# Optimization experiments

Measured on AMD Instinct MI355X. Metric: run time of the kernel, lower is better.

## Reference

```python
import jax, jax.numpy as jnp
import numpy as np

N_HEAD = 16

def setup_inputs() -> dict:
    key = jax.random.key(0)
    ks = jax.random.split(key, 9)
    C = 1024
    s = 1.0 / np.sqrt(C)
    x = jax.random.normal(ks[0], (2, 2048, C), dtype=jnp.float32)
    Wq = jax.random.normal(ks[1], (C, C), dtype=jnp.float32) * s
    Wk = jax.random.normal(ks[2], (C, C), dtype=jnp.float32) * s
    Wv = jax.random.normal(ks[3], (C, C), dtype=jnp.float32) * s
    Wp = jax.random.normal(ks[4], (C, C), dtype=jnp.float32) * s
    z = jnp.zeros((C,), dtype=jnp.float32)
    return {"x": x, "Wq": Wq, "bq": z, "Wk": Wk, "bk": z, "Wv": Wv, "bv": z, "Wp": Wp, "bp": z}

def reference(x, Wq, bq, Wk, bk, Wv, bv, Wp, bp):
    B, T, C = x.shape
    H = N_HEAD
    D = C // H
    # QKV projections (Linear: x @ W.T + b), split heads -> [B, H, T, D]
    q = (x @ Wq.T + bq).reshape(B, T, H, D).transpose(0, 2, 1, 3)
    k = (x @ Wk.T + bk).reshape(B, T, H, D).transpose(0, 2, 1, 3)
    v = (x @ Wv.T + bv).reshape(B, T, H, D).transpose(0, 2, 1, 3)
    scale = 1.0 / jnp.sqrt(jnp.asarray(D, dtype=x.dtype))  # scaled_attn=True
    att = jnp.einsum('bhtd,bhsd->bhts', q, k) * scale      # [B,H,T,T]
    att = jax.nn.softmax(att, axis=-1)
    y = jnp.einsum('bhts,bhsd->bhtd', att, v)              # [B,H,T,D]
    y = y.transpose(0, 2, 1, 3).reshape(B, T, C)
    return y @ Wp.T + bp
```

## Files before the change

kernel.cpp:

```cpp
#include <hip/hip_runtime.h>
#include <stdint.h>

typedef unsigned short u16;
typedef __attribute__((ext_vector_type(8))) short short8;
typedef __attribute__((ext_vector_type(4))) float float4v;
typedef __attribute__((ext_vector_type(4))) u16 ushort4v;
typedef __attribute__((ext_vector_type(2))) unsigned int uint2v;

#define MFMA_BF16(a, b, c) __builtin_amdgcn_mfma_f32_16x16x32_bf16((a), (b), (c), 0, 0, 0)

__device__ __forceinline__ u16 f2bf(float f) {
    uint32_t u = __builtin_bit_cast(uint32_t, f);
    u += 0x7FFFu + ((u >> 16) & 1u);
    return (u16)(u >> 16);
}
__device__ __forceinline__ void g2l16(const void* g, void* l) {
    __builtin_amdgcn_global_load_lds(
        (const __attribute__((address_space(1))) void*)g,
        (__attribute__((address_space(3))) void*)l, 16, 0, 0);
}

__global__ void cast_all(const float* __restrict__ x, const float* __restrict__ wq,
                         const float* __restrict__ wk, const float* __restrict__ wv,
                         const float* __restrict__ wp,
                         u16* __restrict__ xb, u16* __restrict__ wqkvb, u16* __restrict__ wpb) {
    int bx = blockIdx.x;
    const float* src; u16* dst; int base;
    if (bx < 4096)      { src = x;  dst = xb;              base = bx; }
    else if (bx < 5120) { src = wq; dst = wqkvb;           base = bx - 4096; }
    else if (bx < 6144) { src = wk; dst = wqkvb + 1048576; base = bx - 5120; }
    else if (bx < 7168) { src = wv; dst = wqkvb + 2097152; base = bx - 6144; }
    else                { src = wp; dst = wpb;             base = bx - 7168; }
    int i = base * 1024 + threadIdx.x * 4;
    float4v v = *(const float4v*)(src + i);
    ushort4v o;
    #pragma unroll
    for (int r = 0; r < 4; ++r) o[r] = f2bf(v[r]);
    *(ushort4v*)(dst + i) = o;
}

__device__ __forceinline__ void gemm_core_128(const u16* __restrict__ A, const u16* __restrict__ B,
                                              int K, int m0, int n0, float4v acc[4][4]) {
    __shared__ u16 lA[128 * 64];
    __shared__ u16 lB[128 * 64];
    const int tid = threadIdx.x, lane = tid & 63;
    const int wave = tid >> 6, wm = wave >> 1, wn = wave & 1;
    const int l15 = lane & 15, quad = lane >> 4;

    for (int kt = 0; kt < K; kt += 64) {
        __syncthreads();
        #pragma unroll
        for (int i = 0; i < 4; ++i) {
            int f = i * 256 + tid;
            int row = f >> 3, kc = f & 7;
            g2l16(A + (size_t)(m0 + row) * K + kt + kc * 8, &lA[f * 8]);
            g2l16(B + (size_t)(n0 + row) * K + kt + kc * 8, &lB[f * 8]);
        }
        __syncthreads();
        #pragma unroll
        for (int ks = 0; ks < 2; ++ks) {
            short8 af[4], bf[4];
            #pragma unroll
            for (int t = 0; t < 4; ++t) {
                af[t] = *(const short8*)&lA[(wm * 64 + t * 16 + l15) * 64 + ks * 32 + quad * 8];
                bf[t] = *(const short8*)&lB[(wn * 64 + t * 16 + l15) * 64 + ks * 32 + quad * 8];
            }
            #pragma unroll
            for (int tm = 0; tm < 4; ++tm)
                #pragma unroll
                for (int tn = 0; tn < 4; ++tn)
                    acc[tm][tn] = MFMA_BF16(af[tm], bf[tn], acc[tm][tn]);
        }
    }
}

__global__ __launch_bounds__(256, 2) void gemm_qkv(
    const u16* __restrict__ xb, const u16* __restrict__ wqkv,
    const float* __restrict__ bq, const float* __restrict__ bk, const float* __restrict__ bv,
    u16* __restrict__ qo, u16* __restrict__ ko, u16* __restrict__ vto) {
    const int bx = blockIdx.x, by = blockIdx.y;
    const int tid = threadIdx.x, lane = tid & 63;
    const int wave = tid >> 6, wm = wave >> 1, wn = wave & 1;
    const int l15 = lane & 15, quad = lane >> 4;
    const float QSC = 0.125f * 1.44269504088896340736f;

    if (bx < 16) {
        float4v acc[4][4] = {};
        gemm_core_128(wqkv, xb, 1024, bx * 128, by * 128, acc);
        const bool isq = bx < 8;
        const float* bvec = isq ? bq : bk;
        u16* dst = isq ? qo : ko;
        #pragma unroll
        for (int tm = 0; tm < 4; ++tm) {
            int nloc = (bx & 7) * 128 + wm * 64 + tm * 16 + quad * 4;
            int h = nloc >> 6, d0 = nloc & 63;
            float4v bias = *(const float4v*)(bvec + nloc);
            #pragma unroll
            for (int tn = 0; tn < 4; ++tn) {
                int t = by * 128 + wn * 64 + tn * 16 + l15;
                int b = t >> 11, tt = t & 2047;
                ushort4v pk;
                #pragma unroll
                for (int r = 0; r < 4; ++r) {
                    float v = acc[tm][tn][r] + bias[r];
                    pk[r] = f2bf(isq ? v * QSC : v);
                }
                *(ushort4v*)&dst[(((size_t)(b * 16 + h)) * 2048 + tt) * 64 + d0] = pk;
            }
        }
    } else {
        float4v acc[4][4] = {};
        gemm_core_128(xb, wqkv, 1024, by * 128, bx * 128, acc);
        #pragma unroll
        for (int tn = 0; tn < 4; ++tn) {
            int n = bx * 128 + wn * 64 + tn * 16 + l15;
            int cb = n & 1023, h = cb >> 6, d = cb & 63;
            float bias = bv[cb];
            #pragma unroll
            for (int tm = 0; tm < 4; ++tm) {
                int mb = by * 128 + wm * 64 + tm * 16 + quad * 4;
                int b = mb >> 11, t0 = mb & 2047;
                ushort4v pk;
                #pragma unroll
                for (int r = 0; r < 4; ++r) pk[r] = f2bf(acc[tm][tn][r] + bias);
                *(ushort4v*)&vto[(((size_t)(b * 16 + h)) * 64 + d) * 2048 + t0] = pk;
            }
        }
    }
}

__global__ __launch_bounds__(256, 2) void gemm_out(
    const u16* __restrict__ yb, const u16* __restrict__ wpb,
    const float* __restrict__ bp, float* __restrict__ out) {
    float4v acc[4][4] = {};
    gemm_core_128(wpb, yb, 1024, blockIdx.x * 128, blockIdx.y * 128, acc);
    const int tid = threadIdx.x, lane = tid & 63;
    const int wave = tid >> 6, wm = wave >> 1, wn = wave & 1;
    const int l15 = lane & 15, quad = lane >> 4;
    #pragma unroll
    for (int tm = 0; tm < 4; ++tm) {
        int n = blockIdx.x * 128 + wm * 64 + tm * 16 + quad * 4;
        float4v bias = *(const float4v*)(bp + n);
        #pragma unroll
        for (int tn = 0; tn < 4; ++tn) {
            int t = blockIdx.y * 128 + wn * 64 + tn * 16 + l15;
            float4v o;
            #pragma unroll
            for (int r = 0; r < 4; ++r) o[r] = acc[tm][tn][r] + bias[r];
            *(float4v*)&out[(size_t)t * 1024 + n] = o;
        }
    }
}

__global__ __launch_bounds__(256, 2) void attn(
    const u16* __restrict__ qg, const u16* __restrict__ kg,
    const u16* __restrict__ vtg, u16* __restrict__ yb) {
    __shared__ u16 kbuf[128 * 64];
    __shared__ u16 pbuf[128 * 136];
    __shared__ float lsum[2][128];

    const int tid = threadIdx.x, lane = tid & 63;
    const int wave = tid >> 6;
    const int sm = wave >> 1, sn = wave & 1;
    const int mh = wave & 1, nh = wave >> 1;
    const int l15 = lane & 15, quad = lane >> 4;
    const int bh = blockIdx.y, qt0 = blockIdx.x * 128;

    const u16* qbase = qg + (size_t)bh * 2048 * 64;
    const u16* kbase = kg + (size_t)bh * 2048 * 64;
    const u16* vtbase = vtg + (size_t)bh * 64 * 2048;

    short8 qf[4][2];
    #pragma unroll
    for (int tn = 0; tn < 4; ++tn)
        #pragma unroll
        for (int ks = 0; ks < 2; ++ks)
            qf[tn][ks] = *(const short8*)(qbase + (size_t)(qt0 + sn * 64 + tn * 16 + l15) * 64 + ks * 32 + quad * 8);

    float4v oacc[2][4] = {};
    float rs[4] = {};

    for (int it = 0; it < 16; ++it) {
        const int kv0 = it * 128;
        __syncthreads();
        #pragma unroll
        for (int i = 0; i < 4; ++i) {
            int f = i * 256 + tid, row = f >> 3, kc = f & 7;
            g2l16(kbase + (size_t)(kv0 + row) * 64 + kc * 8, &kbuf[f * 8]);
        }
        short8 vf[4][2];
        #pragma unroll
        for (int kst = 0; kst < 4; ++kst)
            #pragma unroll
            for (int tmm = 0; tmm < 2; ++tmm)
                vf[kst][tmm] = *(const short8*)(vtbase + (size_t)(mh * 32 + tmm * 16 + l15) * 2048 + kv0 + kst * 32 + quad * 8);
        __syncthreads();
        float4v sacc[4][4] = {};
        #pragma unroll
        for (int ks = 0; ks < 2; ++ks) {
            short8 kf[4];
            #pragma unroll
            for (int tm = 0; tm < 4; ++tm)
                kf[tm] = *(const short8*)&kbuf[(sm * 64 + tm * 16 + l15) * 64 + ks * 32 + quad * 8];
            #pragma unroll
            for (int tm = 0; tm < 4; ++tm)
                #pragma unroll
                for (int tn = 0; tn < 4; ++tn)
                    sacc[tm][tn] = MFMA_BF16(kf[tm], qf[tn][ks], sacc[tm][tn]);
        }
        #pragma unroll
        for (int tm = 0; tm < 4; ++tm)
            #pragma unroll
            for (int tn = 0; tn < 4; ++tn) {
                uint32_t u[4];
                #pragma unroll
                for (int r = 0; r < 4; ++r) {
                    float p = __builtin_amdgcn_exp2f(sacc[tm][tn][r]);
                    u[r] = __builtin_bit_cast(uint32_t, p);
                    rs[tn] += __builtin_bit_cast(float, u[r] & 0xFFFF0000u);
                }
                uint2v pk;
                pk.x = __builtin_amdgcn_perm(u[1], u[0], 0x07060302u);
                pk.y = __builtin_amdgcn_perm(u[3], u[2], 0x07060302u);
                *(uint2v*)&pbuf[(sn * 64 + tn * 16 + l15) * 136 + sm * 64 + tm * 16 + quad * 4] = pk;
            }
        __syncthreads();
        #pragma unroll
        for (int kst = 0; kst < 4; ++kst) {
            short8 bfn[4];
            #pragma unroll
            for (int tnn = 0; tnn < 4; ++tnn)
                bfn[tnn] = *(const short8*)&pbuf[(nh * 64 + tnn * 16 + l15) * 136 + kst * 32 + quad * 8];
            #pragma unroll
            for (int tmm = 0; tmm < 2; ++tmm)
                #pragma unroll
                for (int tnn = 0; tnn < 4; ++tnn)
                    oacc[tmm][tnn] = MFMA_BF16(vf[kst][tmm], bfn[tnn], oacc[tmm][tnn]);
        }
    }
    #pragma unroll
    for (int tn = 0; tn < 4; ++tn) {
        float v = rs[tn];
        v += __shfl_xor(v, 16);
        v += __shfl_xor(v, 32);
        rs[tn] = v;
    }
    if (lane < 16)
        #pragma unroll
        for (int tn = 0; tn < 4; ++tn)
            lsum[sm][sn * 64 + tn * 16 + l15] = rs[tn];
    __syncthreads();
    const int b = bh >> 4, h = bh & 15;
    #pragma unroll
    for (int tnn = 0; tnn < 4; ++tnn) {
        int qrow = nh * 64 + tnn * 16 + l15;
        float inv = 1.0f / (lsum[0][qrow] + lsum[1][qrow]);
        #pragma unroll
        for (int tmm = 0; tmm < 2; ++tmm) {
            int d0 = mh * 32 + tmm * 16 + quad * 4;
            ushort4v pk;
            #pragma unroll
            for (int r = 0; r < 4; ++r) pk[r] = f2bf(oacc[tmm][tnn][r] * inv);
            *(ushort4v*)&yb[((size_t)(b * 2048 + qt0 + qrow)) * 1024 + h * 64 + d0] = pk;
        }
    }
}

extern "C" void kernel_launch(void* const* d_in, const int* in_sizes, int n_in,
                              void* d_out, int out_size, void* d_ws, size_t ws_size,
                              hipStream_t stream) {
    const float* x  = (const float*)d_in[0];
    const float* Wq = (const float*)d_in[1];
    const float* bq = (const float*)d_in[2];
    const float* Wk = (const float*)d_in[3];
    const float* bk = (const float*)d_in[4];
    const float* Wv = (const float*)d_in[5];
    const float* bv = (const float*)d_in[6];
    const float* Wp = (const float*)d_in[7];
    const float* bp = (const float*)d_in[8];
    float* out = (float*)d_out;
    uint8_t* ws = (uint8_t*)d_ws;

    u16* xb   = (u16*)(ws);
    u16* wqkv = (u16*)(ws + (8u << 20));
    u16* wpb  = (u16*)(ws + (14u << 20));
    u16* qb   = (u16*)(ws + (16u << 20));
    u16* kb   = (u16*)(ws + (24u << 20));
    u16* vtb  = (u16*)(ws + (32u << 20));
    u16* yb   = (u16*)(ws + (40u << 20));

    cast_all<<<8192, 256, 0, stream>>>(x, Wq, Wk, Wv, Wp, xb, wqkv, wpb);
    gemm_qkv<<<dim3(24, 32), 256, 0, stream>>>(xb, wqkv, bq, bk, bv, qb, kb, vtb);
    attn<<<dim3(16, 32), 256, 0, stream>>>(qb, kb, vtb, yb);
    gemm_out<<<dim3(8, 32), 256, 0, stream>>>(yb, wpb, bp, out);
}
```

Baseline: 209.6 us.

## Swizzle LDS tiles and restructure attention into split-KV waves with double buffering

The GEMM core and attention K tile now use an XOR swizzle on the LDS column index to avoid bank conflicts on MFMA fragment reads. The attention kernel shrinks the query tile to 64 rows and doubles the grid. Each wave takes a 32-key slice of every 128-key block, keeps its own P buffer (removing one block barrier per iteration), and double-buffers K loads. Partial outputs are reduced across the four waves through LDS at the end, which adds a final reduction step and more K/V reloads per query.

```diff
diff --git a/kernel.cpp b/kernel.cpp
--- a/kernel.cpp
+++ b/kernel.cpp
@@ -46,6 +46,7 @@
     const int tid = threadIdx.x, lane = tid & 63;
     const int wave = tid >> 6, wm = wave >> 1, wn = wave & 1;
     const int l15 = lane & 15, quad = lane >> 4;
+    const int sw7 = l15 & 7;
 
     for (int kt = 0; kt < K; kt += 64) {
         __syncthreads();
@@ -53,8 +54,9 @@
         for (int i = 0; i < 4; ++i) {
             int f = i * 256 + tid;
             int row = f >> 3, kc = f & 7;
-            g2l16(A + (size_t)(m0 + row) * K + kt + kc * 8, &lA[f * 8]);
-            g2l16(B + (size_t)(n0 + row) * K + kt + kc * 8, &lB[f * 8]);
+            int gcol = (kc ^ (row & 7)) * 8;
+            g2l16(A + (size_t)(m0 + row) * K + kt + gcol, &lA[f * 8]);
+            g2l16(B + (size_t)(n0 + row) * K + kt + gcol, &lB[f * 8]);
         }
         __syncthreads();
         #pragma unroll
@@ -62,8 +64,9 @@
             short8 af[4], bf[4];
             #pragma unroll
             for (int t = 0; t < 4; ++t) {
-                af[t] = *(const short8*)&lA[(wm * 64 + t * 16 + l15) * 64 + ks * 32 + quad * 8];
-                bf[t] = *(const short8*)&lB[(wn * 64 + t * 16 + l15) * 64 + ks * 32 + quad * 8];
+                int pc = ((ks * 4 + quad) ^ sw7) * 8;
+                af[t] = *(const short8*)&lA[(wm * 64 + t * 16 + l15) * 64 + pc];
+                bf[t] = *(const short8*)&lB[(wn * 64 + t * 16 + l15) * 64 + pc];
             }
             #pragma unroll
             for (int tm = 0; tm < 4; ++tm)
@@ -155,61 +158,67 @@
 __global__ __launch_bounds__(256, 2) void attn(
     const u16* __restrict__ qg, const u16* __restrict__ kg,
     const u16* __restrict__ vtg, u16* __restrict__ yb) {
-    __shared__ u16 kbuf[128 * 64];
-    __shared__ u16 pbuf[128 * 136];
-    __shared__ float lsum[2][128];
+    __shared__ __attribute__((aligned(16))) char smem[54272];
+    u16* kb0 = (u16*)smem;
+    u16* pb  = (u16*)(smem + 32768);
+    float* lsum = (float*)(smem + 53248);
+    float* red  = (float*)smem;
 
     const int tid = threadIdx.x, lane = tid & 63;
-    const int wave = tid >> 6;
-    const int sm = wave >> 1, sn = wave & 1;
-    const int mh = wave & 1, nh = wave >> 1;
-    const int l15 = lane & 15, quad = lane >> 4;
-    const int bh = blockIdx.y, qt0 = blockIdx.x * 128;
+    const int w = tid >> 6;
+    const int l15 = lane & 15, quad = lane >> 4, sw7 = l15 & 7;
+    const int bh = blockIdx.y, qt0 = blockIdx.x * 64;
 
     const u16* qbase = qg + (size_t)bh * 2048 * 64;
     const u16* kbase = kg + (size_t)bh * 2048 * 64;
     const u16* vtbase = vtg + (size_t)bh * 64 * 2048;
+    u16* pw = pb + w * 2560;
 
     short8 qf[4][2];
     #pragma unroll
     for (int tn = 0; tn < 4; ++tn)
         #pragma unroll
         for (int ks = 0; ks < 2; ++ks)
-            qf[tn][ks] = *(const short8*)(qbase + (size_t)(qt0 + sn * 64 + tn * 16 + l15) * 64 + ks * 32 + quad * 8);
-
-    float4v oacc[2][4] = {};
+            qf[tn][ks] = *(const short8*)(qbase + (size_t)(qt0 + tn * 16 + l15) * 64 + ks * 32 + quad * 8);
+
+    float4v oacc[4][4] = {};
     float rs[4] = {};
 
-    for (int it = 0; it < 16; ++it) {
-        const int kv0 = it * 128;
-        __syncthreads();
+    {
         #pragma unroll
         for (int i = 0; i < 4; ++i) {
             int f = i * 256 + tid, row = f >> 3, kc = f & 7;
-            g2l16(kbase + (size_t)(kv0 + row) * 64 + kc * 8, &kbuf[f * 8]);
-        }
-        short8 vf[4][2];
-        #pragma unroll
-        for (int kst = 0; kst < 4; ++kst)
-            #pragma unroll
-            for (int tmm = 0; tmm < 2; ++tmm)
-                vf[kst][tmm] = *(const short8*)(vtbase + (size_t)(mh * 32 + tmm * 16 + l15) * 2048 + kv0 + kst * 32 + quad * 8);
+            g2l16(kbase + (size_t)row * 64 + (kc ^ (row & 7)) * 8, &kb0[f * 8]);
+        }
+    }
+
+    for (int it = 0; it < 16; ++it) {
         __syncthreads();
-        float4v sacc[4][4] = {};
+        if (it + 1 < 16) {
+            u16* nb = kb0 + ((it + 1) & 1) * 8192;
+            const u16* src = kbase + (size_t)(it + 1) * 128 * 64;
+            #pragma unroll
+            for (int i = 0; i < 4; ++i) {
+                int f = i * 256 + tid, row = f >> 3, kc = f & 7;
+                g2l16(src + (size_t)row * 64 + (kc ^ (row & 7)) * 8, &nb[f * 8]);
+            }
+        }
+        const u16* kbu = kb0 + (it & 1) * 8192;
+        float4v sacc[2][4] = {};
         #pragma unroll
         for (int ks = 0; ks < 2; ++ks) {
-            short8 kf[4];
-            #pragma unroll
-            for (int tm = 0; tm < 4; ++tm)
-                kf[tm] = *(const short8*)&kbuf[(sm * 64 + tm * 16 + l15) * 64 + ks * 32 + quad * 8];
-            #pragma unroll
-            for (int tm = 0; tm < 4; ++tm)
+            short8 kf[2];
+            #pragma unroll
+            for (int tm = 0; tm < 2; ++tm)
+                kf[tm] = *(const short8*)&kbu[(w * 32 + tm * 16 + l15) * 64 + (((ks * 4 + quad) ^ sw7)) * 8];
+            #pragma unroll
+            for (int tm = 0; tm < 2; ++tm)
                 #pragma unroll
                 for (int tn = 0; tn < 4; ++tn)
                     sacc[tm][tn] = MFMA_BF16(kf[tm], qf[tn][ks], sacc[tm][tn]);
         }
         #pragma unroll
-        for (int tm = 0; tm < 4; ++tm)
+        for (int tm = 0; tm < 2; ++tm)
             #pragma unroll
             for (int tn = 0; tn < 4; ++tn) {
                 uint32_t u[4];
@@ -222,21 +231,21 @@
                 uint2v pk;
                 pk.x = __builtin_amdgcn_perm(u[1], u[0], 0x07060302u);
                 pk.y = __builtin_amdgcn_perm(u[3], u[2], 0x07060302u);
-                *(uint2v*)&pbuf[(sn * 64 + tn * 16 + l15) * 136 + sm * 64 + tm * 16 + quad * 4] = pk;
-            }
-        __syncthreads();
-        #pragma unroll
-        for (int kst = 0; kst < 4; ++kst) {
-            short8 bfn[4];
+                *(uint2v*)&pw[(tn * 16 + l15) * 40 + tm * 16 + quad * 4] = pk;
+            }
+        short8 vf[4];
+        #pragma unroll
+        for (int tmm = 0; tmm < 4; ++tmm)
+            vf[tmm] = *(const short8*)(vtbase + (size_t)(tmm * 16 + l15) * 2048 + it * 128 + w * 32 + quad * 8);
+        short8 bfn[4];
+        #pragma unroll
+        for (int tnn = 0; tnn < 4; ++tnn)
+            bfn[tnn] = *(const short8*)&pw[(tnn * 16 + l15) * 40 + quad * 8];
+        #pragma unroll
+        for (int tmm = 0; tmm < 4; ++tmm)
             #pragma unroll
             for (int tnn = 0; tnn < 4; ++tnn)
-                bfn[tnn] = *(const short8*)&pbuf[(nh * 64 + tnn * 16 + l15) * 136 + kst * 32 + quad * 8];
-            #pragma unroll
-            for (int tmm = 0; tmm < 2; ++tmm)
-                #pragma unroll
-                for (int tnn = 0; tnn < 4; ++tnn)
-                    oacc[tmm][tnn] = MFMA_BF16(vf[kst][tmm], bfn[tnn], oacc[tmm][tnn]);
-        }
+                oacc[tmm][tnn] = MFMA_BF16(vf[tmm], bfn[tnn], oacc[tmm][tnn]);
     }
     #pragma unroll
     for (int tn = 0; tn < 4; ++tn) {
@@ -248,20 +257,44 @@
     if (lane < 16)
         #pragma unroll
         for (int tn = 0; tn < 4; ++tn)
-            lsum[sm][sn * 64 + tn * 16 + l15] = rs[tn];
+            lsum[w * 64 + tn * 16 + l15] = rs[tn];
     __syncthreads();
-    const int b = bh >> 4, h = bh & 15;
-    #pragma unroll
-    for (int tnn = 0; tnn < 4; ++tnn) {
-        int qrow = nh * 64 + tnn * 16 + l15;
-        float inv = 1.0f / (lsum[0][qrow] + lsum[1][qrow]);
-        #pragma unroll
-        for (int tmm = 0; tmm < 2; ++tmm) {
-            int d0 = mh * 32 + tmm * 16 + quad * 4;
-            ushort4v pk;
-            #pragma unroll
-            for (int r = 0; r < 4; ++r) pk[r] = f2bf(oacc[tmm][tnn][r] * inv);
-            *(ushort4v*)&yb[((size_t)(b * 2048 + qt0 + qrow)) * 1024 + h * 64 + d0] = pk;
+    if (w > 0) {
+        float* dst = red + (w - 1) * 4096;
+        #pragma unroll
+        for (int tmm = 0; tmm < 4; ++tmm)
+            #pragma unroll
+            for (int tnn = 0; tnn < 4; ++tnn)
+                *(float4v*)&dst[((tmm * 4 + tnn) * 64 + lane) * 4] = oacc[tmm][tnn];
+    }
+    __syncthreads();
+    if (w == 0) {
+        const int b = bh >> 4, h = bh & 15;
+        #pragma unroll
+        for (int tmm = 0; tmm < 4; ++tmm)
+            #pragma unroll
+            for (int tnn = 0; tnn < 4; ++tnn) {
+                float4v s = oacc[tmm][tnn];
+                #pragma unroll
+                for (int ww = 0; ww < 3; ++ww) {
+                    float4v o = *(const float4v*)&red[(ww * 4096) + ((tmm * 4 + tnn) * 64 + lane) * 4];
+                    #pragma unroll
+                    for (int r = 0; r < 4; ++r) s[r] += o[r];
+                }
+                oacc[tmm][tnn] = s;
+            }
+        #pragma unroll
+        for (int tnn = 0; tnn < 4; ++tnn) {
+            int q = tnn * 16 + l15;
+            float inv = 1.0f / (lsum[q] + lsum[64 + q] + lsum[128 + q] + lsum[192 + q]);
+            #pragma unroll
+            for (int tmm = 0; tmm < 4; ++tmm) {
+                int d0 = tmm * 16 + quad * 4;
+                ushort4v pk;
+                #pragma unroll
+                for (int r = 0; r < 4; ++r) pk[r] = f2bf(oacc[tmm][tnn][r] * inv);
+                *(ushort4v*)&yb[((size_t)(b * 2048 + qt0 + q)) * 1024 + h * 64 + d0] = pk;
+            }
         }
     }
 }
@@ -291,6 +324,6 @@
 
     cast_all<<<8192, 256, 0, stream>>>(x, Wq, Wk, Wv, Wp, xb, wqkv, wpb);
     gemm_qkv<<<dim3(24, 32), 256, 0, stream>>>(xb, wqkv, bq, bk, bv, qb, kb, vtb);
-    attn<<<dim3(16, 32), 256, 0, stream>>>(qb, kb, vtb, yb);
+    attn<<<dim3(32, 32), 256, 0, stream>>>(qb, kb, vtb, yb);
     gemm_out<<<dim3(8, 32), 256, 0, stream>>>(yb, wpb, bp, out);
 }
```

Measured after the change: 196.5 us. 1.07x faster.
